# Kernel tuning notes

Measured on AMD Instinct MI355X. Metric: run time of the kernel, lower is better.

Reference implementation:

```python
import jax, jax.numpy as jnp
import numpy as np

ALPHA = 0.01  # LeakyReLU negative slope

def _leaky(x):
    return jnp.where(x > 0, x, ALPHA * x)

def _conv(x, w, b):
    # x: NHWC, w: HWIO, valid padding, stride 1
    return jax.lax.conv_general_dilated(x, w, (1, 1), 'VALID',
        dimension_numbers=('NHWC', 'HWIO', 'NHWC')) + b

def _maxpool2(x):
    return jax.lax.reduce_window(x, -jnp.inf, jax.lax.max,
        (1, 2, 2, 1), (1, 2, 2, 1), 'VALID')

def setup_inputs() -> dict:
    key = jax.random.key(0)
    ks = jax.random.split(key, 32)
    B, S, H = 32, 197, 256
    FLAT = 47 * 62 * 64  # after conv/pool trunk = 186496
    def w(k, shape, fan_in):
        return jax.random.normal(k, shape, dtype=jnp.float32) * np.float32(1.0 / np.sqrt(fan_in))
    inp = {
        'x': jax.random.normal(ks[0], (B, S, H), dtype=jnp.float32),
        'conv1_w': w(ks[1], (3, 3, 1, 32), 9), 'conv1_b': jnp.zeros((32,), jnp.float32),
        'conv2_w': w(ks[2], (3, 3, 32, 64), 288), 'conv2_b': jnp.zeros((64,), jnp.float32),
        'w_c1': w(ks[3], (FLAT, 512), FLAT), 'b_c1': jnp.zeros((512,), jnp.float32),
        'w_c2': w(ks[4], (512, 256), 512), 'b_c2': jnp.zeros((256,), jnp.float32),
        'w_co': w(ks[5], (256, 225 * 13), 256), 'b_co': jnp.zeros((225 * 13,), jnp.float32),
        'w_sm': w(ks[6], (13, 13), 13), 'b_sm': jnp.zeros((13,), jnp.float32),
        'w_r1': w(ks[7], (FLAT, 256), FLAT), 'b_r1': jnp.zeros((256,), jnp.float32),
        'w_r2': w(ks[8], (256, 128), 256), 'b_r2': jnp.zeros((128,), jnp.float32),
        'w_r3': w(ks[9], (128, 128), 128), 'b_r3': jnp.zeros((128,), jnp.float32),
        'w_r4': w(ks[10], (128, 64), 128), 'b_r4': jnp.zeros((64,), jnp.float32),
        'w_ro': w(ks[11], (64, 225 * 4), 64), 'b_ro': jnp.zeros((225 * 4,), jnp.float32),
        'w_sg': w(ks[12], (4, 4), 4), 'b_sg': jnp.zeros((4,), jnp.float32),
    }
    return inp

def reference(x, conv1_w, conv1_b, conv2_w, conv2_b,
              w_c1, b_c1, w_c2, b_c2, w_co, b_co, w_sm, b_sm,
              w_r1, b_r1, w_r2, b_r2, w_r3, b_r3, w_r4, b_r4,
              w_ro, b_ro, w_sg, b_sg):
    # CNN trunk on expanded hidden state (B, S, H, 1)
    h = x[..., None]
    h = jax.nn.relu(_conv(h, conv1_w, conv1_b))
    h = _maxpool2(h)
    h = jax.nn.relu(_conv(h, conv2_w, conv2_b))
    h = _maxpool2(h)
    h = h.reshape(h.shape[0], -1)  # (B, 186496)
    # classification branch (dropout is identity at inference)
    y = _leaky(h @ w_c1 + b_c1)
    y = _leaky(y @ w_c2 + b_c2)
    y = _leaky(y @ w_co + b_co).reshape(-1, 225, 13)
    # 225-step loop of shared Dense(13, softmax) heads -> one batched matmul
    class_out = jax.nn.softmax(jnp.einsum('bpi,ij->bpj', y, w_sm) + b_sm, axis=-1)
    z = _leaky(h @ w_r1 + b_r1)
    z = _leaky(z @ w_r2 + b_r2)
    z = _leaky(z @ w_r3 + b_r3)
    z = _leaky(z @ w_r4 + b_r4)
    z = (z @ w_ro + b_ro).reshape(-1, 225, 4)
    reg_out = jax.nn.sigmoid(jnp.einsum('bpi,ij->bpj', z, w_sg) + b_sg)
    return class_out, reg_out
```

## Files before the change

kernel.cpp:

```cpp
#include <hip/hip_runtime.h>
#include <hip/hip_bf16.h>

#define ALPHA 0.01f

typedef __attribute__((ext_vector_type(8))) __bf16 bf16x8;
typedef __attribute__((ext_vector_type(4))) float f32x4;

#define BATCH 32
#define P1H 97
#define P1W 127
#define P2W 62
#define FLAT 186496
#define GK 512
#define NGK 365
#define PSTRIDE1 16448
#define PSTRIDE2 8256
#define CONV1_BLOCKS 1540
#define LPITCH 264

static __device__ __forceinline__ unsigned short f2bf(float x) {
  union { float f; unsigned u; } c; c.f = x;
  unsigned r = c.u + 0x7fffu + ((c.u >> 16) & 1u);
  return (unsigned short)(r >> 16);
}

static __device__ __forceinline__ unsigned pack2bf(float lo, float hi) {
  union { float f; unsigned u; } a, b;
  a.f = lo; b.f = hi;
  unsigned ra = (a.u + 0x7fffu + ((a.u >> 16) & 1u)) >> 16;
  unsigned rb = (b.u + 0x7fffu + ((b.u >> 16) & 1u)) & 0xffff0000u;
  return ra | rb;
}

__global__ __launch_bounds__(256) void conv1_pool(const float* __restrict__ x,
    const float* __restrict__ w1, const float* __restrict__ b1,
    unsigned short* __restrict__ p1,
    const float* __restrict__ w2, unsigned short* __restrict__ bpack) {
  if (blockIdx.x >= CONV1_BLOCKS) {
    int o = (blockIdx.x - CONV1_BLOCKS) * 256 + threadIdx.x;
    if (o < 9 * 4 * 512) {
      int f = o >> 9;
      int within = o & 511;
      int lane = within >> 3, j = within & 7;
      int tap = f >> 2, nf = f & 3;
      int k = ((lane >> 4) << 3) + j;
      int n = nf * 16 + (lane & 15);
      bpack[o] = f2bf(w2[(tap * 32 + k) * 64 + n]);
    }
    return;
  }
  int pid = blockIdx.x * 256 + threadIdx.x;
  if (pid >= BATCH * P1H * P1W) return;
  int b = pid / (P1H * P1W);
  int rem = pid - b * (P1H * P1W);
  int ph = rem / P1W;
  int pw = rem - ph * P1W;
  const float* xb = x + ((b * 197 + 2 * ph) * 256 + 2 * pw);
  float in[4][4];
#pragma unroll
  for (int r = 0; r < 4; ++r) {
    float2 v0 = *reinterpret_cast<const float2*>(xb + r * 256);
    float2 v1 = *reinterpret_cast<const float2*>(xb + r * 256 + 2);
    in[r][0] = v0.x; in[r][1] = v0.y; in[r][2] = v1.x; in[r][3] = v1.y;
  }
  unsigned pk[16];
#pragma unroll
  for (int c = 0; c < 32; ++c) {
    float s00 = b1[c], s01 = s00, s10 = s00, s11 = s00;
#pragma unroll
    for (int ky = 0; ky < 3; ++ky)
#pragma unroll
      for (int kx = 0; kx < 3; ++kx) {
        float w = w1[(ky * 3 + kx) * 32 + c];
        s00 = fmaf(in[ky][kx], w, s00);
        s01 = fmaf(in[ky][kx + 1], w, s01);
        s10 = fmaf(in[ky + 1][kx], w, s10);
        s11 = fmaf(in[ky + 1][kx + 1], w, s11);
      }
    float m = fmaxf(fmaxf(s00, s01), fmaxf(s10, s11));
    m = fmaxf(m, 0.0f);
    unsigned short u = f2bf(m);
    if (c & 1) pk[c >> 1] |= ((unsigned)u) << 16;
    else pk[c >> 1] = (unsigned)u;
  }
  uint4* dst = reinterpret_cast<uint4*>(p1 + (size_t)pid * 32);
#pragma unroll
  for (int g = 0; g < 4; ++g)
    dst[g] = make_uint4(pk[g * 4], pk[g * 4 + 1], pk[g * 4 + 2], pk[g * 4 + 3]);
}

__global__ __launch_bounds__(256) void conv2_pool(const unsigned short* __restrict__ p1,
    const unsigned short* __restrict__ bpack, const float* __restrict__ b2,
    unsigned short* __restrict__ hbf) {
  __shared__ alignas(16) unsigned char lds_buf[65536];
  int prow = blockIdx.x, b = blockIdx.y;
  int tid = threadIdx.x;
  int lane = tid & 63, wid = tid >> 6;
  {
    const uint4* src = reinterpret_cast<const uint4*>(bpack);
    uint4* dst = reinterpret_cast<uint4*>(lds_buf);
    for (int i = tid; i < 2304; i += 256) dst[i] = src[i];
  }
  __syncthreads();
  int row = lane & 15, kg = lane >> 4;
  int rowbase[4];
  int coff[4][3];
#pragma unroll
  for (int mf = 0; mf < 4; ++mf) {
    int m = wid * 64 + mf * 16 + row;
    int cro = m >> 7, cc = m & 127;
    rowbase[mf] = ((b * 97 + 2 * prow + cro) * 127) * 32 + kg * 8;
#pragma unroll
    for (int kx = 0; kx < 3; ++kx) {
      int ic = cc + kx; if (ic > 126) ic = 126;
      coff[mf][kx] = ic * 32;
    }
  }
  f32x4 acc[4][4];
#pragma unroll
  for (int i = 0; i < 4; ++i)
#pragma unroll
    for (int j = 0; j < 4; ++j) acc[i][j] = (f32x4){0.f, 0.f, 0.f, 0.f};

  const bf16x8* bl = reinterpret_cast<const bf16x8*>(lds_buf);
#pragma unroll
  for (int ky = 0; ky < 3; ++ky) {
#pragma unroll
    for (int kx = 0; kx < 3; ++kx) {
      int tap = ky * 3 + kx;
      bf16x8 a[4];
#pragma unroll
      for (int mf = 0; mf < 4; ++mf) {
        int addr = rowbase[mf] + ky * (127 * 32) + coff[mf][kx];
        a[mf] = *reinterpret_cast<const bf16x8*>(p1 + addr);
      }
      bf16x8 bf[4];
#pragma unroll
      for (int nf = 0; nf < 4; ++nf) bf[nf] = bl[(tap * 4 + nf) * 64 + lane];
#pragma unroll
      for (int nf = 0; nf < 4; ++nf)
#pragma unroll
        for (int mf = 0; mf < 4; ++mf)
          acc[mf][nf] = __builtin_amdgcn_mfma_f32_16x16x32_bf16(a[mf], bf[nf], acc[mf][nf], 0, 0, 0);
    }
  }
  __syncthreads();
  float* stage = reinterpret_cast<float*>(lds_buf);
#pragma unroll
  for (int mf = 0; mf < 4; ++mf)
#pragma unroll
    for (int nf = 0; nf < 4; ++nf) {
      int ch = nf * 16 + (lane & 15);
      float bias = b2[ch];
#pragma unroll
      for (int j = 0; j < 4; ++j) {
        int m = wid * 64 + mf * 16 + (lane >> 4) * 4 + j;
        float v = acc[mf][nf][j] + bias;
        stage[m * 64 + ch] = fmaxf(v, 0.f);
      }
    }
  __syncthreads();
  unsigned short* hb = hbf + (size_t)b * FLAT + prow * (P2W * 64);
  for (int o = tid; o < P2W * 64; o += 256) {
    int pw = o >> 6, ch = o & 63;
    int c0 = 2 * pw;
    float v = fmaxf(fmaxf(stage[c0 * 64 + ch], stage[(c0 + 1) * 64 + ch]),
                    fmaxf(stage[(128 + c0) * 64 + ch], stage[(129 + c0) * 64 + ch]));
    hb[o] = f2bf(v);
  }
}

template <int N, int CSTRIDE>
__global__ __launch_bounds__(256) void gemm_mfma(const float* __restrict__ W,
    const unsigned short* __restrict__ hbf, float* __restrict__ part) {
  __shared__ alignas(16) unsigned lds[16 * LPITCH];
  int kc = blockIdx.y;
  int n0 = blockIdx.x * 256;
  int t = threadIdx.x, lane = t & 63, w = t >> 6;
  int k0 = kc * GK;
  int klen = FLAT - k0; if (klen > GK) klen = GK;
  int nsteps = klen >> 5;
  int cl = lane & 15, kg = lane >> 4;
  int mh = w & 1, nh = w >> 1;

  const float* wsrc = W + (size_t)(k0 + w * 8) * N + n0 + lane * 4;
  unsigned* lwb = lds + (w * 4) * LPITCH + lane * 4;
  const unsigned short* ha = hbf + (size_t)(mh * 16 + cl) * FLAT + k0 + kg * 8;

  f32x4 acc[8];
#pragma unroll
  for (int f = 0; f < 8; ++f) acc[f] = (f32x4){0.f, 0.f, 0.f, 0.f};

  float4 st[8];
#pragma unroll
  for (int i = 0; i < 8; ++i)
    st[i] = *reinterpret_cast<const float4*>(wsrc + (size_t)i * N);

  for (int kt = 0; kt < nsteps; ++kt) {
    __syncthreads();
#pragma unroll
    for (int ip = 0; ip < 4; ++ip) {
      float4 lo = st[2 * ip], hi = st[2 * ip + 1];
      *reinterpret_cast<uint4*>(lwb + ip * LPITCH) =
          make_uint4(pack2bf(lo.x, hi.x), pack2bf(lo.y, hi.y),
                     pack2bf(lo.z, hi.z), pack2bf(lo.w, hi.w));
    }
    __syncthreads();
    if (kt + 1 < nsteps) {
      const float* ws = wsrc + (size_t)(kt + 1) * 32 * N;
#pragma unroll
      for (int i = 0; i < 8; ++i)
        st[i] = *reinterpret_cast<const float4*>(ws + (size_t)i * N);
    }
    bf16x8 a = *reinterpret_cast<const bf16x8*>(ha + kt * 32);
#pragma unroll
    for (int f = 0; f < 8; ++f) {
      int col = nh * 128 + f * 16 + cl;
      union { unsigned u[4]; bf16x8 v; } bb;
#pragma unroll
      for (int p = 0; p < 4; ++p)
        bb.u[p] = lds[(kg * 4 + p) * LPITCH + col];
      acc[f] = __builtin_amdgcn_mfma_f32_16x16x32_bf16(a, bb.v, acc[f], 0, 0, 0);
    }
  }

  float* out = part + (size_t)kc * CSTRIDE + n0;
#pragma unroll
  for (int f = 0; f < 8; ++f)
#pragma unroll
    for (int j = 0; j < 4; ++j) {
      int m = mh * 16 + kg * 4 + j;
      int col = nh * 128 + f * 16 + cl;
      out[m * N + col] = acc[f][j];
    }
}

__global__ __launch_bounds__(256) void reduce_big(const float* __restrict__ part1,
    const float* __restrict__ part2, const float* __restrict__ b_c1,
    const float* __restrict__ b_r1, float* __restrict__ y1, float* __restrict__ z1) {
  __shared__ float red[8][32];
  int b = blockIdx.x, t = threadIdx.x;
  int oo = t & 31, j = t >> 5;
  float s = 0.f;
  if (b < 512) {
    const float* p = part1 + b * 32 + oo;
    for (int c = j; c < NGK; c += 8) s += p[(size_t)c * PSTRIDE1];
    red[j][oo] = s;
    __syncthreads();
    if (t < 32) {
      float r = 0.f;
#pragma unroll
      for (int jj = 0; jj < 8; ++jj) r += red[jj][t];
      int o = b * 32 + t;
      r += b_c1[o & 511];
      y1[o] = r > 0.f ? r : ALPHA * r;
    }
  } else {
    const float* p = part2 + (b - 512) * 32 + oo;
    for (int c = j; c < NGK; c += 8) s += p[(size_t)c * PSTRIDE2];
    red[j][oo] = s;
    __syncthreads();
    if (t < 32) {
      float r = 0.f;
#pragma unroll
      for (int jj = 0; jj < 8; ++jj) r += red[jj][t];
      int u = (b - 512) * 32 + t;
      r += b_r1[u & 255];
      z1[u] = r > 0.f ? r : ALPHA * r;
    }
  }
}

__global__ __launch_bounds__(256) void tail_all(
    const float* __restrict__ y1g, const float* __restrict__ z1g,
    const float* __restrict__ w_c2, const float* __restrict__ b_c2,
    const float* __restrict__ w_co, const float* __restrict__ b_co,
    const float* __restrict__ w_sm, const float* __restrict__ b_sm,
    const float* __restrict__ w_r2, const float* __restrict__ b_r2,
    const float* __restrict__ w_r3, const float* __restrict__ b_r3,
    const float* __restrict__ w_r4, const float* __restrict__ b_r4,
    const float* __restrict__ w_ro, const float* __restrict__ b_ro,
    const float* __restrict__ w_sg, const float* __restrict__ b_sg,
    float* __restrict__ class_out, float* __restrict__ reg_out) {
  int tile = blockIdx.x, m = blockIdx.y, t = threadIdx.x;
  if (tile < 8) {
    __shared__ float ly1[512], ly2[256], ly3[29 * 13];
    ly1[t] = y1g[m * 512 + t];
    ly1[t + 256] = y1g[m * 512 + 256 + t];
    __syncthreads();
    {
      float s = b_c2[t];
      for (int k = 0; k < 512; ++k) s = fmaf(ly1[k], w_c2[k * 256 + t], s);
      ly2[t] = s > 0.f ? s : ALPHA * s;
    }
    __syncthreads();
    int p0 = tile * 29;
    int np = 225 - p0; if (np > 29) np = 29;
    int ncols = np * 13;
    for (int n = t; n < ncols; n += 256) {
      int col = p0 * 13 + n;
      float s = b_co[col];
      for (int k = 0; k < 256; ++k) s = fmaf(ly2[k], w_co[k * 2925 + col], s);
      ly3[n] = s > 0.f ? s : ALPHA * s;
    }
    __syncthreads();
    if (t < np) {
      float v[13], l[13], mx = -1e30f;
#pragma unroll
      for (int i = 0; i < 13; ++i) v[i] = ly3[t * 13 + i];
#pragma unroll
      for (int j = 0; j < 13; ++j) {
        float s = b_sm[j];
#pragma unroll
        for (int i = 0; i < 13; ++i) s = fmaf(v[i], w_sm[i * 13 + j], s);
        l[j] = s; mx = fmaxf(mx, s);
      }
      float sum = 0.f;
#pragma unroll
      for (int j = 0; j < 13; ++j) { l[j] = expf(l[j] - mx); sum += l[j]; }
      float inv = 1.f / sum;
      float* o = class_out + ((size_t)m * 225 + p0 + t) * 13;
#pragma unroll
      for (int j = 0; j < 13; ++j) o[j] = l[j] * inv;
    }
  } else {
    __shared__ float lz1[256], lz2[128], lz3[128], lz4[64], lzo[57 * 4];
    lz1[t] = z1g[m * 256 + t];
    __syncthreads();
    if (t < 128) {
      float s = b_r2[t];
      for (int k = 0; k < 256; ++k) s = fmaf(lz1[k], w_r2[k * 128 + t], s);
      lz2[t] = s > 0.f ? s : ALPHA * s;
    }
    __syncthreads();
    if (t < 128) {
      float s = b_r3[t];
      for (int k = 0; k < 128; ++k) s = fmaf(lz2[k], w_r3[k * 128 + t], s);
      lz3[t] = s > 0.f ? s : ALPHA * s;
    }
    __syncthreads();
    if (t < 64) {
      float s = b_r4[t];
      for (int k = 0; k < 128; ++k) s = fmaf(lz3[k], w_r4[k * 64 + t], s);
      lz4[t] = s > 0.f ? s : ALPHA * s;
    }
    __syncthreads();
    int p0 = (tile - 8) * 57;
    int np = 225 - p0; if (np > 57) np = 57;
    int ncols = np * 4;
    for (int n = t; n < ncols; n += 256) {
      int col = p0 * 4 + n;
      float s = b_ro[col];
#pragma unroll
      for (int k = 0; k < 64; ++k) s = fmaf(lz4[k], w_ro[k * 900 + col], s);
      lzo[n] = s;
    }
    __syncthreads();
    if (t < np) {
      float z[4];
#pragma unroll
      for (int i = 0; i < 4; ++i) z[i] = lzo[t * 4 + i];
      float* ro = reg_out + ((size_t)m * 225 + p0 + t) * 4;
#pragma unroll
      for (int j = 0; j < 4; ++j) {
        float s = b_sg[j];
#pragma unroll
        for (int i = 0; i < 4; ++i) s = fmaf(z[i], w_sg[i * 4 + j], s);
        ro[j] = 1.f / (1.f + expf(-s));
      }
    }
  }
}

#define OFF_P1     ((size_t)0)
#define OFF_BPACK  ((size_t)25229312)
#define OFF_H      ((size_t)25266176)
#define OFF_PART1  ((size_t)37201920)
#define OFF_PART2  ((size_t)61216000)
#define OFF_Y1     ((size_t)73269760)
#define OFF_Z1     ((size_t)73335296)

extern "C" void kernel_launch(void* const* d_in, const int* in_sizes, int n_in,
                              void* d_out, int out_size, void* d_ws, size_t ws_size,
                              hipStream_t stream) {
  const float* x     = (const float*)d_in[0];
  const float* w1    = (const float*)d_in[1];
  const float* b1    = (const float*)d_in[2];
  const float* w2    = (const float*)d_in[3];
  const float* b2    = (const float*)d_in[4];
  const float* w_c1  = (const float*)d_in[5];
  const float* b_c1  = (const float*)d_in[6];
  const float* w_c2  = (const float*)d_in[7];
  const float* b_c2  = (const float*)d_in[8];
  const float* w_co  = (const float*)d_in[9];
  const float* b_co  = (const float*)d_in[10];
  const float* w_sm  = (const float*)d_in[11];
  const float* b_sm  = (const float*)d_in[12];
  const float* w_r1  = (const float*)d_in[13];
  const float* b_r1  = (const float*)d_in[14];
  const float* w_r2  = (const float*)d_in[15];
  const float* b_r2  = (const float*)d_in[16];
  const float* w_r3  = (const float*)d_in[17];
  const float* b_r3  = (const float*)d_in[18];
  const float* w_r4  = (const float*)d_in[19];
  const float* b_r4  = (const float*)d_in[20];
  const float* w_ro  = (const float*)d_in[21];
  const float* b_ro  = (const float*)d_in[22];
  const float* w_sg  = (const float*)d_in[23];
  const float* b_sg  = (const float*)d_in[24];

  char* ws = (char*)d_ws;
  unsigned short* p1    = (unsigned short*)(ws + OFF_P1);
  unsigned short* bpack = (unsigned short*)(ws + OFF_BPACK);
  unsigned short* hbf   = (unsigned short*)(ws + OFF_H);
  float*          part1 = (float*)(ws + OFF_PART1);
  float*          part2 = (float*)(ws + OFF_PART2);
  float*          y1    = (float*)(ws + OFF_Y1);
  float*          z1    = (float*)(ws + OFF_Z1);

  float* class_out = (float*)d_out;
  float* reg_out   = (float*)d_out + 32 * 225 * 13;

  conv1_pool<<<CONV1_BLOCKS + 72, 256, 0, stream>>>(x, w1, b1, p1, w2, bpack);
  conv2_pool<<<dim3(47, 32), 256, 0, stream>>>(p1, bpack, b2, hbf);
  gemm_mfma<512, PSTRIDE1><<<dim3(2, NGK), 256, 0, stream>>>(w_c1, hbf, part1);
  gemm_mfma<256, PSTRIDE2><<<dim3(1, NGK), 256, 0, stream>>>(w_r1, hbf, part2);
  reduce_big<<<768, 256, 0, stream>>>(part1, part2, b_c1, b_r1, y1, z1);
  tail_all<<<dim3(12, 32), 256, 0, stream>>>(y1, z1,
      w_c2, b_c2, w_co, b_co, w_sm, b_sm,
      w_r2, b_r2, w_r3, b_r3, w_r4, b_r4,
      w_ro, b_ro, w_sg, b_sg, class_out, reg_out);
}
```

Baseline: 257.1 us.

## Merge both big GEMMs into one launch with double-buffered LDS pipeline

Measured after the change: 416.6 us. 62.0% more time.

```diff
diff --git a/kernel.cpp b/kernel.cpp
--- a/kernel.cpp
+++ b/kernel.cpp
@@ -16,7 +16,7 @@
 #define PSTRIDE1 16448
 #define PSTRIDE2 8256
 #define CONV1_BLOCKS 1540
-#define LPITCH 264
+#define LPITCH 266
 
 static __device__ __forceinline__ unsigned short f2bf(float x) {
   union { float f; unsigned u; } c; c.f = x;
@@ -170,61 +170,84 @@
   }
 }
 
-template <int N, int CSTRIDE>
-__global__ __launch_bounds__(256) void gemm_mfma(const float* __restrict__ W,
-    const unsigned short* __restrict__ hbf, float* __restrict__ part) {
-  __shared__ alignas(16) unsigned lds[16 * LPITCH];
-  int kc = blockIdx.y;
-  int n0 = blockIdx.x * 256;
+__global__ __launch_bounds__(256, 4) void gemm_mfma(
+    const float* __restrict__ w_c1, const float* __restrict__ w_r1,
+    const unsigned short* __restrict__ hbf,
+    float* __restrict__ part1, float* __restrict__ part2) {
+  __shared__ alignas(16) unsigned lds[2][16 * LPITCH];
+  int py = blockIdx.x, kc = blockIdx.y;
+  const float* W; int N, n0, cstride; float* pbase;
+  if (py < 2) { W = w_c1; N = 512; n0 = py * 256; pbase = part1; cstride = PSTRIDE1; }
+  else        { W = w_r1; N = 256; n0 = 0;        pbase = part2; cstride = PSTRIDE2; }
   int t = threadIdx.x, lane = t & 63, w = t >> 6;
   int k0 = kc * GK;
   int klen = FLAT - k0; if (klen > GK) klen = GK;
   int nsteps = klen >> 5;
   int cl = lane & 15, kg = lane >> 4;
   int mh = w & 1, nh = w >> 1;
+  size_t kstep = (size_t)32 * N;
 
   const float* wsrc = W + (size_t)(k0 + w * 8) * N + n0 + lane * 4;
-  unsigned* lwb = lds + (w * 4) * LPITCH + lane * 4;
+  unsigned* lwb0 = &lds[0][(w * 4) * LPITCH + lane * 4];
+  unsigned* lwb1 = &lds[1][(w * 4) * LPITCH + lane * 4];
   const unsigned short* ha = hbf + (size_t)(mh * 16 + cl) * FLAT + k0 + kg * 8;
 
   f32x4 acc[8];
 #pragma unroll
   for (int f = 0; f < 8; ++f) acc[f] = (f32x4){0.f, 0.f, 0.f, 0.f};
 
-  float4 st[8];
-#pragma unroll
-  for (int i = 0; i < 8; ++i)
-    st[i] = *reinterpret_cast<const float4*>(wsrc + (size_t)i * N);
-
-  for (int kt = 0; kt < nsteps; ++kt) {
-    __syncthreads();
-#pragma unroll
-    for (int ip = 0; ip < 4; ++ip) {
-      float4 lo = st[2 * ip], hi = st[2 * ip + 1];
-      *reinterpret_cast<uint4*>(lwb + ip * LPITCH) =
-          make_uint4(pack2bf(lo.x, hi.x), pack2bf(lo.y, hi.y),
-                     pack2bf(lo.z, hi.z), pack2bf(lo.w, hi.w));
-    }
-    __syncthreads();
-    if (kt + 1 < nsteps) {
-      const float* ws = wsrc + (size_t)(kt + 1) * 32 * N;
-#pragma unroll
-      for (int i = 0; i < 8; ++i)
-        st[i] = *reinterpret_cast<const float4*>(ws + (size_t)i * N);
-    }
-    bf16x8 a = *reinterpret_cast<const bf16x8*>(ha + kt * 32);
-#pragma unroll
-    for (int f = 0; f < 8; ++f) {
-      int col = nh * 128 + f * 16 + cl;
-      union { unsigned u[4]; bf16x8 v; } bb;
-#pragma unroll
-      for (int p = 0; p < 4; ++p)
-        bb.u[p] = lds[(kg * 4 + p) * LPITCH + col];
-      acc[f] = __builtin_amdgcn_mfma_f32_16x16x32_bf16(a, bb.v, acc[f], 0, 0, 0);
-    }
-  }
-
-  float* out = part + (size_t)kc * CSTRIDE + n0;
+  float4 sA[8], sB[8];
+
+#define LOAD8(dst, ptr)                                                        \
+  _Pragma("unroll") for (int i_ = 0; i_ < 8; ++i_)                             \
+    dst[i_] = *reinterpret_cast<const float4*>((ptr) + (size_t)i_ * N);
+
+#define PACK8(src, lwb)                                                        \
+  _Pragma("unroll") for (int ip_ = 0; ip_ < 4; ++ip_) {                        \
+    float4 lo_ = src[2 * ip_], hi_ = src[2 * ip_ + 1];                         \
+    *reinterpret_cast<uint4*>((lwb) + ip_ * LPITCH) =                          \
+        make_uint4(pack2bf(lo_.x, hi_.x), pack2bf(lo_.y, hi_.y),               \
+                   pack2bf(lo_.z, hi_.z), pack2bf(lo_.w, hi_.w));              \
+  }
+
+#define MFMA8(buf, areg)                                                       \
+  _Pragma("unroll") for (int f_ = 0; f_ < 8; ++f_) {                           \
+    int col_ = nh * 128 + f_ * 16 + cl;                                        \
+    union { unsigned u[4]; bf16x8 v; } bb_;                                    \
+    _Pragma("unroll") for (int p_ = 0; p_ < 4; ++p_)                           \
+      bb_.u[p_] = (buf)[(kg * 4 + p_) * LPITCH + col_];                        \
+    acc[f_] = __builtin_amdgcn_mfma_f32_16x16x32_bf16(areg, bb_.v, acc[f_], 0, 0, 0); \
+  }
+
+  LOAD8(sA, wsrc);
+  LOAD8(sB, wsrc + kstep);
+  PACK8(sA, lwb0);
+  bf16x8 a_cur = *reinterpret_cast<const bf16x8*>(ha);
+  const float* wissue = wsrc + 2 * kstep;
+
+  for (int kt = 0; kt < nsteps; kt += 2) {
+    __syncthreads();
+    if (kt + 2 < nsteps) { LOAD8(sA, wissue); }
+    bf16x8 a0 = a_cur;
+    if (kt + 1 < nsteps)
+      a_cur = *reinterpret_cast<const bf16x8*>(ha + (kt + 1) * 32);
+    MFMA8(lds[0], a0);
+    PACK8(sB, lwb1);
+    wissue += kstep;
+    __syncthreads();
+    if (kt + 3 < nsteps) { LOAD8(sB, wissue); }
+    bf16x8 a1 = a_cur;
+    if (kt + 2 < nsteps)
+      a_cur = *reinterpret_cast<const bf16x8*>(ha + (kt + 2) * 32);
+    MFMA8(lds[1], a1);
+    if (kt + 2 < nsteps) { PACK8(sA, lwb0); }
+    wissue += kstep;
+  }
+#undef LOAD8
+#undef PACK8
+#undef MFMA8
+
+  float* out = pbase + (size_t)kc * cstride + n0;
 #pragma unroll
   for (int f = 0; f < 8; ++f)
 #pragma unroll
@@ -423,8 +446,7 @@
 
   conv1_pool<<<CONV1_BLOCKS + 72, 256, 0, stream>>>(x, w1, b1, p1, w2, bpack);
   conv2_pool<<<dim3(47, 32), 256, 0, stream>>>(p1, bpack, b2, hbf);
-  gemm_mfma<512, PSTRIDE1><<<dim3(2, NGK), 256, 0, stream>>>(w_c1, hbf, part1);
-  gemm_mfma<256, PSTRIDE2><<<dim3(1, NGK), 256, 0, stream>>>(w_r1, hbf, part2);
+  gemm_mfma<<<dim3(3, NGK), 256, 0, stream>>>(w_c1, w_r1, hbf, part1, part2);
   reduce_big<<<768, 256, 0, stream>>>(part1, part2, b_c1, b_r1, y1, z1);
   tail_all<<<dim3(12, 32), 256, 0, stream>>>(y1, z1,
       w_c2, b_c2, w_co, b_co, w_sm, b_sm,
```
